# Kernel tuning notes

Measured on AMD Instinct MI355X. Metric: run time of the kernel, lower is better.

## Reference

```python
import jax, jax.numpy as jnp
import numpy as np

N = 10000   # nodes
E = 100000  # edges
B = 64      # graphs
HID = 128


def setup_inputs() -> dict:
    key = jax.random.key(0)
    ks = iter(jax.random.split(key, 64))
    def nrm(shape, s=0.1):
        return jax.random.normal(next(ks), shape, dtype=jnp.float32) * s
    inp = {}
    inp["x"] = nrm((N, 1), 1.0)
    inp["node_type"] = jax.random.randint(next(ks), (N,), 0, 2)
    inp["edge_index"] = jax.random.randint(next(ks), (2, E), 0, N)
    inp["edge_attr"] = nrm((E, 1), 1.0)
    inp["batch"] = jnp.sort(jax.random.randint(next(ks), (N,), 0, B))
    inp["vp_w"] = nrm((1, HID)); inp["vp_b"] = nrm((HID,))
    inp["type_emb"] = nrm((2, HID))
    def conv(pre, fin, h, c):
        inp[pre + "_wl"] = nrm((fin, h * c)); inp[pre + "_bl"] = nrm((h * c,))
        inp[pre + "_wr"] = nrm((fin, h * c)); inp[pre + "_br"] = nrm((h * c,))
        inp[pre + "_we"] = nrm((1, h * c));  inp[pre + "_att"] = nrm((h, c))
        inp[pre + "_bias"] = nrm((h * c if pre != "c3" else c,))
    conv("c1", HID, 8, HID)
    conv("c2", HID * 8, 2, HID)
    conv("c3", HID * 2, 1, HID)
    inp["m1_w"] = nrm((HID, HID)); inp["m1_b"] = nrm((HID,))
    inp["ln1_g"] = jnp.ones((HID,), jnp.float32); inp["ln1_b"] = jnp.zeros((HID,), jnp.float32)
    inp["m2_w"] = nrm((HID, HID // 2)); inp["m2_b"] = nrm((HID // 2,))
    inp["ln2_g"] = jnp.ones((HID // 2,), jnp.float32); inp["ln2_b"] = jnp.zeros((HID // 2,), jnp.float32)
    inp["m3_w"] = nrm((HID // 2, 1)); inp["m3_b"] = nrm((1,))
    return inp


def _gatv2(x, src, dst, ea, wl, bl, wr, br, we, att, bias, heads, out_ch, concat):
    """PyG GATv2Conv (eval mode): add self-loops (edge_attr fill='mean' over dst),
    attn = (att * leaky_relu(Wl x_src + Wr x_dst + We e)).sum(-1), segment-softmax
    over destination, scatter-add of alpha * Wl x_src."""
    n = x.shape[0]
    ones = jnp.ones((ea.shape[0], 1), ea.dtype)
    deg = jax.ops.segment_sum(ones, dst, num_segments=n)
    loop_attr = jax.ops.segment_sum(ea, dst, num_segments=n) / jnp.maximum(deg, 1.0)
    ar = jnp.arange(n, dtype=src.dtype)
    src2 = jnp.concatenate([src, ar])
    dst2 = jnp.concatenate([dst, ar])
    ea2 = jnp.concatenate([ea, loop_attr], axis=0)
    xl = (x @ wl + bl).reshape(n, heads, out_ch)   # source transform
    xr = (x @ wr + br).reshape(n, heads, out_ch)   # target transform
    e = (ea2 @ we).reshape(-1, heads, out_ch)      # [E2, H, C]
    msg = xl[src2]                                 # [E2, H, C]
    z = jax.nn.leaky_relu(msg + xr[dst2] + e, 0.2)
    score = jnp.einsum('ehc,hc->eh', z, att)       # [E2, H]
    smax = jax.ops.segment_max(score, dst2, num_segments=n)
    ex = jnp.exp(score - smax[dst2])
    denom = jax.ops.segment_sum(ex, dst2, num_segments=n)
    alpha = ex / denom[dst2]
    out = jax.ops.segment_sum(alpha[:, :, None] * msg, dst2, num_segments=n)
    out = out.reshape(n, heads * out_ch) if concat else out.mean(axis=1)
    return out + bias


def _layernorm(v, g, b):
    mu = v.mean(-1, keepdims=True)
    var = v.var(-1, keepdims=True)
    return (v - mu) / jnp.sqrt(var + 1e-5) * g + b


def reference(x, node_type, edge_index, edge_attr, batch,
              vp_w, vp_b, type_emb,
              c1_wl, c1_bl, c1_wr, c1_br, c1_we, c1_att, c1_bias,
              c2_wl, c2_bl, c2_wr, c2_br, c2_we, c2_att, c2_bias,
              c3_wl, c3_bl, c3_wr, c3_br, c3_we, c3_att, c3_bias,
              m1_w, m1_b, ln1_g, ln1_b, m2_w, m2_b, ln2_g, ln2_b, m3_w, m3_b):
    src, dst = edge_index[0], edge_index[1]
    h = x @ vp_w + vp_b + type_emb[node_type]
    h = jax.nn.leaky_relu(_gatv2(h, src, dst, edge_attr, c1_wl, c1_bl, c1_wr, c1_br, c1_we, c1_att, c1_bias, 8, HID, True), 0.2)
    h = jax.nn.leaky_relu(_gatv2(h, src, dst, edge_attr, c2_wl, c2_bl, c2_wr, c2_br, c2_we, c2_att, c2_bias, 2, HID, True), 0.2)
    h = jax.nn.leaky_relu(_gatv2(h, src, dst, edge_attr, c3_wl, c3_bl, c3_wr, c3_br, c3_we, c3_att, c3_bias, 1, HID, False), 0.2)
    # masked global mean pool over node_type == 0
    w = (node_type == 0).astype(h.dtype)
    sums = jax.ops.segment_sum(h * w[:, None], batch, num_segments=B)
    cnts = jax.ops.segment_sum(w, batch, num_segments=B)
    pooled = sums / jnp.maximum(cnts, 1.0)[:, None]
    h1 = jax.nn.leaky_relu(_layernorm(pooled @ m1_w + m1_b, ln1_g, ln1_b), 0.2)
    h2 = jax.nn.leaky_relu(_layernorm(h1 @ m2_w + m2_b, ln2_g, ln2_b), 0.2)
    return (h2 @ m3_w + m3_b).squeeze(-1)
```

## Files before the change

kernel.cpp:

```cpp
#include <hip/hip_runtime.h>
#include <math.h>

#define NN 10000
#define NE 100000
#define NBATCH 64

typedef short bf16x8 __attribute__((ext_vector_type(8)));
typedef float f32x4 __attribute__((ext_vector_type(4)));

__device__ __forceinline__ float lrelu(float v){ return fmaxf(v, 0.2f*v); }

__device__ __forceinline__ unsigned short f2bf(float x){
  unsigned int u = __float_as_uint(x);
  u += 0x7fffu + ((u >> 16) & 1u);
  return (unsigned short)(u >> 16);
}
__device__ __forceinline__ float bf2f(unsigned short u){
  return __uint_as_float(((unsigned int)u) << 16);
}

__global__ __launch_bounds__(256) void prep_kernel(
    const float* __restrict__ vp_w, const float* __restrict__ vp_b,
    const float* __restrict__ type_emb,
    const float* __restrict__ c1_wl, const float* __restrict__ c1_bl,
    const float* __restrict__ c1_wr, const float* __restrict__ c1_br,
    float* __restrict__ Ul, float* __restrict__ CTl,
    float* __restrict__ Ur, float* __restrict__ CTr,
    const float* __restrict__ c2_wl, const float* __restrict__ c2_wr,
    const float* __restrict__ c3_wl, const float* __restrict__ c3_wr,
    unsigned short* __restrict__ W2lT, unsigned short* __restrict__ W2rT,
    unsigned short* __restrict__ W3lT, unsigned short* __restrict__ W3rT,
    float* __restrict__ zbase, int zero_words)
{
  __shared__ float t[64][65];
  int b = blockIdx.x;
  int tid = threadIdx.x;
  if (b < 144){
    const float* in; unsigned short* out; int K, N, idx;
    if (b < 64)      { in=c2_wl; out=W2lT; K=1024; N=256; idx=b; }
    else if (b <128) { in=c2_wr; out=W2rT; K=1024; N=256; idx=b-64; }
    else if (b <136) { in=c3_wl; out=W3lT; K=256;  N=128; idx=b-128; }
    else             { in=c3_wr; out=W3rT; K=256;  N=128; idx=b-136; }
    int K64 = K >> 6;
    int kx = idx % K64, nx = idx / K64;
    int k0 = kx*64, n0 = nx*64;
    int lr = tid >> 4;
    int lc = (tid & 15) * 4;
#pragma unroll
    for (int i=0;i<4;++i){
      int r = lr + i*16;
      float4 v = *(const float4*)(in + (size_t)(k0+r)*N + n0 + lc);
      t[r][lc+0]=v.x; t[r][lc+1]=v.y; t[r][lc+2]=v.z; t[r][lc+3]=v.w;
    }
    __syncthreads();
    int sr = tid >> 3;
    int sc = (tid & 7) * 8;
#pragma unroll
    for (int i=0;i<2;++i){
      int n = sr + i*32;
      unsigned short tmp[8];
#pragma unroll
      for (int j=0;j<8;++j) tmp[j] = f2bf(t[sc+j][n]);
      unsigned short* op = out + (size_t)(n0+n)*K + k0 + sc;
      *(ushort4*)op       = make_ushort4(tmp[0],tmp[1],tmp[2],tmp[3]);
      *(ushort4*)(op + 4) = make_ushort4(tmp[4],tmp[5],tmp[6],tmp[7]);
    }
  } else if (b < 148){
    int j = (b-144)*256 + tid;
    float ul=0.f, c0l=0.f, c1l=0.f, ur=0.f, c0r=0.f, c1r=0.f;
    for (int k=0; k<128; ++k){
      float a = c1_wl[k*1024 + j], bb = c1_wr[k*1024 + j];
      float vw = vp_w[k], vb = vp_b[k], t0 = type_emb[k], t1 = type_emb[128+k];
      ul += vw*a; ur += vw*bb;
      c0l += (vb+t0)*a; c1l += (vb+t1)*a;
      c0r += (vb+t0)*bb; c1r += (vb+t1)*bb;
    }
    float bl = c1_bl[j], br = c1_br[j];
    Ul[j]=ul; Ur[j]=ur;
    CTl[j]      = c0l + bl;
    CTl[1024+j] = c1l + bl;
    CTr[j]      = c0r + br;
    CTr[1024+j] = c1r + br;
  } else {
    for (int i = (b-148)*256 + tid; i < zero_words; i += 32*256)
      zbase[i] = 0.f;
  }
}

__global__ void count_kernel(const int* __restrict__ dst, const float* __restrict__ ea,
                             int* __restrict__ deg, float* __restrict__ loop_sum){
  int e = blockIdx.x*256 + threadIdx.x;
  if (e < NE){
    int d = dst[e];
    atomicAdd(&deg[d], 1);
    atomicAdd(&loop_sum[d], ea[e]);
  }
}

__global__ __launch_bounds__(1024) void scan_kernel(const int* __restrict__ deg,
    const float* __restrict__ loop_sum, const float* __restrict__ x,
    const int* __restrict__ ntype,
    int* __restrict__ rowptr, float* __restrict__ loop_attr, float2* __restrict__ xt){
  __shared__ int wtot[16];
  int tid = threadIdx.x;
  int lane = tid & 63, wid = tid >> 6;
  int base = tid*10;
  int d[10]; int run = 0;
#pragma unroll
  for (int j=0;j<10;++j){
    int i = base + j;
    int v = (i < NN) ? deg[i] : 0;
    run += v; d[j] = run;
  }
  int T = run;
  int incl = T;
#pragma unroll
  for (int off=1; off<64; off<<=1){
    int s = __shfl_up(incl, off, 64);
    if (lane >= off) incl += s;
  }
  if (lane == 63) wtot[wid] = incl;
  __syncthreads();
  int wpre = 0;
  for (int w2=0; w2<wid; ++w2) wpre += wtot[w2];
  int ebase = wpre + incl - T;
#pragma unroll
  for (int j=0;j<10;++j){
    int i = base + j;
    if (i < NN){
      int v = d[j] - ((j==0) ? 0 : d[j-1]);
      rowptr[i] = ebase + d[j] - v;
      loop_attr[i] = loop_sum[i] / fmaxf((float)v, 1.f);
      xt[i] = make_float2(x[i], (float)ntype[i]);
    }
  }
  if (tid == 1023) rowptr[NN] = wpre + incl;
}

__global__ void fill_kernel(const int* __restrict__ src, const int* __restrict__ dst,
                            const float* __restrict__ ea, const int* __restrict__ rowptr,
                            int* __restrict__ rowctr, int2* __restrict__ se){
  int e = blockIdx.x*256 + threadIdx.x;
  if (e < NE){
    int d = dst[e];
    int p = rowptr[d] + atomicAdd(&rowctr[d], 1);
    se[p] = make_int2(src[e], __float_as_int(ea[e]));
  }
}

__global__ __launch_bounds__(256) void conv1_fused(
    const int* __restrict__ rowptr, const int2* __restrict__ se,
    const float* __restrict__ loop_attr, const float2* __restrict__ xt,
    const float* __restrict__ Ul, const float* __restrict__ Ur,
    const float* __restrict__ CTl, const float* __restrict__ CTr,
    const float* __restrict__ we, const float* __restrict__ att,
    const float* __restrict__ bias, unsigned short* __restrict__ out)
{
  int n = blockIdx.x*2 + (threadIdx.x >> 7);
  if (n >= NN) return;
  int te = threadIdx.x & 127;
  int ch0 = te * 8;
  float ul[8], wev[8], atv[8], cn0[8], cnd[8];
#pragma unroll
  for (int v=0; v<8; ++v){ ul[v]=Ul[ch0+v]; wev[v]=we[ch0+v]; atv[v]=att[ch0+v]; }
  int beg = rowptr[n], deg = rowptr[n+1]-beg;
  float2 xtn = xt[n];
  float la = loop_attr[n];
  const float* ctr = (xtn.y != 0.f) ? (CTr+1024) : CTr;
#pragma unroll
  for (int v=0; v<8; ++v){
    float c0 = CTl[ch0+v], c1 = CTl[1024+ch0+v];
    cn0[v] = fmaf(xtn.x, Ur[ch0+v], ctr[ch0+v]) + c0;
    cnd[v] = c1 - c0;
  }
  const int2* sp = se + beg;
  const int2 self = make_int2(n, __float_as_int(la));
  int2 qc = (deg > 0) ? sp[0] : self;
  float2 xc = xt[qc.x];
  int2 qn = (1 < deg) ? sp[1] : self;
  float l = 0.f, s1 = 0.f, st1 = 0.f;
  for (int idx=0; idx<=deg; ++idx){
    int2 qnn = (idx+2 < deg) ? sp[idx+2] : self;
    float2 xn = xt[qn.x];
    float xs = xc.x, tf = xc.y, ea = __int_as_float(qc.y);
    float acc = 0.f;
#pragma unroll
    for (int v=0; v<8; ++v){
      float t = fmaf(tf, cnd[v], cn0[v]);
      float z = fmaf(xs, ul[v], fmaf(ea, wev[v], t));
      acc = fmaf(atv[v], fmaxf(z, 0.2f*z), acc);
    }
    acc += __shfl_xor(acc, 1, 16);
    acc += __shfl_xor(acc, 2, 16);
    acc += __shfl_xor(acc, 4, 16);
    acc += __shfl_xor(acc, 8, 16);
    float pe = __expf(acc);
    l += pe;
    s1  = fmaf(pe, xs, s1);
    st1 = fmaf(pe, tf, st1);
    qc = qn; xc = xn; qn = qnn;
  }
  float inv = 1.f/l;
  s1 *= inv;
  float s21 = st1 * inv;
  float s20 = 1.f - s21;
  bf16x8 ov;
#pragma unroll
  for (int v=0; v<8; ++v){
    float c0 = CTl[ch0+v], c1 = CTl[1024+ch0+v];
    float o = lrelu(fmaf(s1, ul[v], fmaf(s20, c0, fmaf(s21, c1, bias[ch0+v]))));
    ov[v] = (short)f2bf(o);
  }
  *(bf16x8*)(out + (size_t)n*1024 + ch0) = ov;
}

template<int H, int NPB, int VPT, bool ONLY0, bool OUTBF, bool INBF>
__global__ __launch_bounds__(64*NPB) void conv_kernel(
    const int* __restrict__ rowptr, const int2* __restrict__ se,
    const float* __restrict__ loop_attr, const int* __restrict__ ntype,
    const void* __restrict__ Xv, int stride, int xr_off,
    const float* __restrict__ we, const float* __restrict__ att, const float* __restrict__ bias,
    void* __restrict__ out)
{
  const int HC = 64*VPT;
  const int TPH = 64/H;
  int n = blockIdx.x*NPB + (threadIdx.x >> 6);
  if (n >= NN) return;
  if (ONLY0 && ntype[n] != 0) return;
  int tid = threadIdx.x & 63;
  int ch0 = tid * VPT;
  const float* Xf = (const float*)Xv;
  const unsigned short* Xb = (const unsigned short*)Xv;
  float wev[VPT], atv[VPT], biv[VPT], xrv[VPT];
#pragma unroll
  for (int v=0; v<VPT; ++v){
    int ch = ch0+v;
    wev[v]=we[ch]; atv[v]=att[ch]; biv[v]=bias[ch];
  }
  if constexpr (INBF){
    ushort4 q = *(const ushort4*)(Xb + (size_t)n*stride + xr_off + ch0);
    xrv[0]=bf2f(q.x); xrv[1]=bf2f(q.y); xrv[2]=bf2f(q.z); xrv[3]=bf2f(q.w);
  } else {
#pragma unroll
    for (int v=0; v<VPT; ++v) xrv[v]=Xf[(size_t)n*stride + xr_off + ch0+v];
  }
  float ls[4], A[4][VPT];
#pragma unroll
  for (int k=0; k<4; ++k){
    ls[k] = 0.f;
#pragma unroll
    for (int v=0; v<VPT; ++v) A[k][v] = 0.f;
  }
  int beg=rowptr[n], end=rowptr[n+1];
  float la = loop_attr[n];
  for (int j=beg; j<=end; j+=4){
    bool val[4]; int sx[4]; float ex[4];
#pragma unroll
    for (int k=0; k<4; ++k){
      int pos = j + k;
      val[k] = pos <= end;
      int2 q;
      if (pos < end) q = se[pos];
      else           q = make_int2(n, __float_as_int(la));
      sx[k] = q.x; ex[k] = __int_as_float(q.y);
    }
    float xv[4][VPT];
#pragma unroll
    for (int k=0; k<4; ++k){
      if constexpr (INBF){
        ushort4 q = *(const ushort4*)(Xb + (size_t)sx[k]*stride + ch0);
        xv[k][0]=bf2f(q.x); xv[k][1]=bf2f(q.y); xv[k][2]=bf2f(q.z); xv[k][3]=bf2f(q.w);
      } else if constexpr (VPT == 4){
        float4 q = *(const float4*)(Xf + (size_t)sx[k]*stride + ch0);
        xv[k][0]=q.x; xv[k][1]=q.y; xv[k][2]=q.z; xv[k][3]=q.w;
      } else {
        float2 q = *(const float2*)(Xf + (size_t)sx[k]*stride + ch0);
        xv[k][0]=q.x; xv[k][1]=q.y;
      }
    }
    float p[4];
#pragma unroll
    for (int k=0; k<4; ++k){
      float acc = 0.f;
#pragma unroll
      for (int v=0; v<VPT; ++v)
        acc += atv[v]*lrelu(xv[k][v]+xrv[v]+ex[k]*wev[v]);
      p[k] = acc;
    }
#pragma unroll
    for (int mm=1; mm<TPH; mm<<=1){
#pragma unroll
      for (int k=0; k<4; ++k) p[k] += __shfl_xor(p[k], mm, 64);
    }
#pragma unroll
    for (int k=0; k<4; ++k){
      float pe = val[k] ? __expf(p[k]) : 0.f;
      ls[k] += pe;
#pragma unroll
      for (int v=0; v<VPT; ++v) A[k][v] = fmaf(pe, xv[k][v], A[k][v]);
    }
  }
  float lt = (ls[0]+ls[1]) + (ls[2]+ls[3]);
  float inv = 1.f/lt;
  size_t baseo=(size_t)n*HC+ch0;
  if constexpr (OUTBF){
    unsigned short* ob = (unsigned short*)out;
    ushort4 o;
    o.x = f2bf(lrelu(((A[0][0]+A[1][0])+(A[2][0]+A[3][0]))*inv+biv[0]));
    o.y = f2bf(lrelu(((A[0][1]+A[1][1])+(A[2][1]+A[3][1]))*inv+biv[1]));
    o.z = f2bf(lrelu(((A[0][2]+A[1][2])+(A[2][2]+A[3][2]))*inv+biv[2]));
    o.w = f2bf(lrelu(((A[0][3]+A[1][3])+(A[2][3]+A[3][3]))*inv+biv[3]));
    *(ushort4*)(ob + baseo) = o;
  } else {
    float* of = (float*)out;
#pragma unroll
    for (int v=0; v<VPT; ++v)
      of[baseo+v] = lrelu(((A[0][v]+A[1][v])+(A[2][v]+A[3][v]))*inv+biv[v]);
  }
}

template<bool OUTBF>
__global__ __launch_bounds__(256) void gemm_dual_lds(
    const short* __restrict__ Abf,
    const short* __restrict__ WlT, const short* __restrict__ WrT,
    const float* __restrict__ bl, const float* __restrict__ br,
    void* __restrict__ Out, int M, int K, int NcH, int cgrid, int rgrid)
{
  __shared__ short lds[12288];
  int id = blockIdx.x;
  int xcd = id & 7, slot = id >> 3;
  int nb = slot % cgrid;
  int rowgroup = (slot / cgrid) * 8 + xcd;
  if (rowgroup >= rgrid) return;
  int row0 = rowgroup * 128;
  int NC2 = 2*NcH;
  int halfx = NcH >> 6;
  int isR = nb >= halfx;
  const short* WT = isR ? WrT : WlT;
  const float* bias = isR ? br : bl;
  int col0 = (nb - (isR ? halfx : 0)) * 64;
  int gcol0 = nb * 64;
  int tid = threadIdx.x;
  int lane = tid & 63, wave = tid >> 6;
  int wm = wave >> 1, wn = wave & 1;
  int quad = lane >> 4, l16 = lane & 15;

  const short* asrc[4];
#pragma unroll
  for (int i=0;i<4;++i){
    int c = wave*256 + i*64 + lane;
    int m = c >> 3, j = c & 7;
    int gr = row0 + m; gr = gr < M ? gr : M-1;
    asrc[i] = Abf + (size_t)gr*K + ((j ^ (m & 7)) << 3);
  }
  const short* bsrc[2];
#pragma unroll
  for (int i=0;i<2;++i){
    int c = wave*128 + i*64 + lane;
    int nloc = c >> 3, j = c & 7;
    bsrc[i] = WT + (size_t)(col0 + nloc)*K + ((j ^ (nloc & 7)) << 3);
  }

  float biasv[2] = { bias[col0 + wn*32 + l16], bias[col0 + wn*32 + 16 + l16] };
  f32x4 acc[4][2];
#pragma unroll
  for (int f=0; f<4; ++f)
#pragma unroll
    for (int g=0; g<2; ++g) acc[f][g] = (f32x4){0.f,0.f,0.f,0.f};

  int niter = K >> 6;
  for (int it=0; it<niter; ++it){
    int k0 = it << 6;
#pragma unroll
    for (int i=0;i<4;++i)
      __builtin_amdgcn_global_load_lds(asrc[i] + k0, &lds[(wave*256 + i*64)*8], 16, 0, 0);
#pragma unroll
    for (int i=0;i<2;++i)
      __builtin_amdgcn_global_load_lds(bsrc[i] + k0, &lds[8192 + (wave*128 + i*64)*8], 16, 0, 0);
    __syncthreads();
#pragma unroll
    for (int s=0; s<2; ++s){
      int t = s*4 + quad;
      bf16x8 af[4], bfv[2];
#pragma unroll
      for (int f=0; f<4; ++f){
        int m = wm*64 + f*16 + l16;
        af[f] = *(const bf16x8*)&lds[m*64 + ((t ^ (m & 7)) << 3)];
      }
#pragma unroll
      for (int g=0; g<2; ++g){
        int nloc = wn*32 + g*16 + l16;
        bfv[g] = *(const bf16x8*)&lds[8192 + nloc*64 + ((t ^ (nloc & 7)) << 3)];
      }
#pragma unroll
      for (int f=0; f<4; ++f)
#pragma unroll
        for (int g=0; g<2; ++g)
          acc[f][g] = __builtin_amdgcn_mfma_f32_16x16x32_bf16(af[f], bfv[g], acc[f][g], 0,0,0);
    }
    __syncthreads();
  }

#pragma unroll
  for (int f=0; f<4; ++f){
    int rbase = row0 + wm*64 + f*16 + quad*4;
#pragma unroll
    for (int r=0; r<4; ++r){
      int rr = rbase + r;
      if (rr < M){
#pragma unroll
        for (int g=0; g<2; ++g){
          int cc = gcol0 + wn*32 + g*16 + l16;
          float val = acc[f][g][r] + biasv[g];
          if constexpr (OUTBF) ((unsigned short*)Out)[(size_t)rr*NC2 + cc] = f2bf(val);
          else                 ((float*)Out)[(size_t)rr*NC2 + cc] = val;
        }
      }
    }
  }
}

__device__ __forceinline__ int lbound(const int* __restrict__ a, int n, int key){
  int lo = 0, hi = n;
  while (lo < hi){ int mid = (lo+hi) >> 1; if (a[mid] < key) lo = mid+1; else hi = mid; }
  return lo;
}

__global__ __launch_bounds__(128) void head_kernel(
    const float* __restrict__ h3, const int* __restrict__ ntype, const int* __restrict__ batch,
    const float* __restrict__ m1w, const float* __restrict__ m1b,
    const float* __restrict__ g1, const float* __restrict__ b1,
    const float* __restrict__ m2w, const float* __restrict__ m2b,
    const float* __restrict__ g2, const float* __restrict__ b2,
    const float* __restrict__ m3w, const float* __restrict__ m3b,
    float* __restrict__ out)
{
  __shared__ float p[128];
  __shared__ float hb[128];
  __shared__ float red[128];
  int b = blockIdx.x, j = threadIdx.x;
  int lo = lbound(batch, NN, b);
  int hi = lbound(batch, NN, b+1);
  float s = 0.f, cnt = 0.f;
  int n = lo;
  for (; n + 3 < hi; n += 4){
    float w0 = (ntype[n]   == 0) ? 1.f : 0.f;
    float w1 = (ntype[n+1] == 0) ? 1.f : 0.f;
    float w2 = (ntype[n+2] == 0) ? 1.f : 0.f;
    float w3 = (ntype[n+3] == 0) ? 1.f : 0.f;
    s += w0*h3[(size_t)n*128 + j]     + w1*h3[(size_t)(n+1)*128 + j]
       + w2*h3[(size_t)(n+2)*128 + j] + w3*h3[(size_t)(n+3)*128 + j];
    cnt += w0 + w1 + w2 + w3;
  }
  for (; n < hi; ++n){
    float w = (ntype[n] == 0) ? 1.f : 0.f;
    s += w*h3[(size_t)n*128 + j];
    cnt += w;
  }
  p[j] = s / fmaxf(cnt, 1.f);
  __syncthreads();
  float a = m1b[j];
  for (int k=0; k<128; ++k) a += p[k]*m1w[k*128 + j];
  red[j] = a; __syncthreads();
  for (int off=64; off>0; off>>=1){ if (j<off) red[j] += red[j+off]; __syncthreads(); }
  float mu = red[0] * (1.f/128.f);
  __syncthreads();
  float d = a - mu;
  red[j] = d*d; __syncthreads();
  for (int off=64; off>0; off>>=1){ if (j<off) red[j] += red[j+off]; __syncthreads(); }
  float var = red[0] * (1.f/128.f);
  __syncthreads();
  hb[j] = lrelu(d * rsqrtf(var + 1e-5f) * g1[j] + b1[j]);
  __syncthreads();
  float a2 = 0.f;
  if (j < 64){
    a2 = m2b[j];
    for (int k=0; k<128; ++k) a2 += hb[k]*m2w[k*64 + j];
  }
  red[j] = (j<64) ? a2 : 0.f; __syncthreads();
  for (int off=64; off>0; off>>=1){ if (j<off) red[j] += red[j+off]; __syncthreads(); }
  float mu2 = red[0] * (1.f/64.f);
  __syncthreads();
  float d2 = a2 - mu2;
  red[j] = (j<64) ? d2*d2 : 0.f; __syncthreads();
  for (int off=64; off>0; off>>=1){ if (j<off) red[j] += red[j+off]; __syncthreads(); }
  float var2 = red[0] * (1.f/64.f);
  __syncthreads();
  if (j < 64) hb[j] = lrelu(d2 * rsqrtf(var2 + 1e-5f) * g2[j] + b2[j]);
  __syncthreads();
  if (j == 0){
    float o = m3b[0];
    for (int k=0; k<64; ++k) o += hb[k]*m3w[k];
    out[b] = o;
  }
}

extern "C" void kernel_launch(void* const* d_in, const int* in_sizes, int n_in,
                              void* d_out, int out_size, void* d_ws, size_t ws_size,
                              hipStream_t stream)
{
  const float* x        = (const float*)d_in[0];
  const int*   ntype    = (const int*)d_in[1];
  const int*   ei       = (const int*)d_in[2];
  const float* eattr    = (const float*)d_in[3];
  const int*   batch    = (const int*)d_in[4];
  const float* vp_w     = (const float*)d_in[5];
  const float* vp_b     = (const float*)d_in[6];
  const float* type_emb = (const float*)d_in[7];
  const float* c1_wl = (const float*)d_in[8];  const float* c1_bl = (const float*)d_in[9];
  const float* c1_wr = (const float*)d_in[10]; const float* c1_br = (const float*)d_in[11];
  const float* c1_we = (const float*)d_in[12]; const float* c1_att= (const float*)d_in[13];
  const float* c1_bias=(const float*)d_in[14];
  const float* c2_wl = (const float*)d_in[15]; const float* c2_bl = (const float*)d_in[16];
  const float* c2_wr = (const float*)d_in[17]; const float* c2_br = (const float*)d_in[18];
  const float* c2_we = (const float*)d_in[19]; const float* c2_att= (const float*)d_in[20];
  const float* c2_bias=(const float*)d_in[21];
  const float* c3_wl = (const float*)d_in[22]; const float* c3_bl = (const float*)d_in[23];
  const float* c3_wr = (const float*)d_in[24]; const float* c3_br = (const float*)d_in[25];
  const float* c3_we = (const float*)d_in[26]; const float* c3_att= (const float*)d_in[27];
  const float* c3_bias=(const float*)d_in[28];
  const float* m1_w = (const float*)d_in[29]; const float* m1_b = (const float*)d_in[30];
  const float* ln1_g= (const float*)d_in[31]; const float* ln1_b= (const float*)d_in[32];
  const float* m2_w = (const float*)d_in[33]; const float* m2_b = (const float*)d_in[34];
  const float* ln2_g= (const float*)d_in[35]; const float* ln2_b= (const float*)d_in[36];
  const float* m3_w = (const float*)d_in[37]; const float* m3_b = (const float*)d_in[38];
  const int* esrc = ei;
  const int* edst = ei + NE;
  float* outp = (float*)d_out;
  (void)in_sizes; (void)n_in; (void)out_size; (void)ws_size;

  char* w = (char*)d_ws;
  auto alloc = [&](size_t bytes) -> void* {
    void* p = (void*)w;
    w += (bytes + 255) & ~(size_t)255;
    return p;
  };
  unsigned short* h1bf = (unsigned short*)alloc((size_t)NN*1024*2);
  unsigned short* X2   = (unsigned short*)alloc((size_t)NN*512*2);
  unsigned short* h2bf = (unsigned short*)alloc((size_t)NN*256*2);
  float* X3   = (float*)alloc((size_t)NN*256*4);
  float* h3   = (float*)alloc((size_t)NN*128*4);
  unsigned short* W2lT = (unsigned short*)alloc((size_t)256*1024*2);
  unsigned short* W2rT = (unsigned short*)alloc((size_t)256*1024*2);
  unsigned short* W3lT = (unsigned short*)alloc((size_t)128*256*2);
  unsigned short* W3rT = (unsigned short*)alloc((size_t)128*256*2);
  float* Ul   = (float*)alloc(1024*4);
  float* CTl  = (float*)alloc(2048*4);
  float* Ur   = (float*)alloc(1024*4);
  float* CTr  = (float*)alloc(2048*4);
  const int zero_words = 3*NN;
  float* zbase = (float*)alloc((size_t)zero_words*4);
  int*   deg      = (int*)zbase;
  int*   rowctr   = (int*)(zbase + NN);
  float* loop_sum = zbase + 2*NN;
  float* loop_attr= (float*)alloc((size_t)NN*4);
  float2* xt      = (float2*)alloc((size_t)NN*8);
  int*   rowptr   = (int*)alloc((size_t)(NN+1)*4);
  int2*  se       = (int2*)alloc((size_t)NE*8);

  prep_kernel<<<180, 256, 0, stream>>>(vp_w, vp_b, type_emb,
      c1_wl, c1_bl, c1_wr, c1_br, Ul, CTl, Ur, CTr,
      c2_wl, c2_wr, c3_wl, c3_wr, W2lT, W2rT, W3lT, W3rT,
      zbase, zero_words);
  count_kernel<<<(NE+255)/256, 256, 0, stream>>>(edst, eattr, deg, loop_sum);
  scan_kernel<<<1, 1024, 0, stream>>>(deg, loop_sum, x, ntype, rowptr, loop_attr, xt);
  fill_kernel<<<(NE+255)/256, 256, 0, stream>>>(esrc, edst, eattr, rowptr, rowctr, se);
  conv1_fused<<<NN/2, 256, 0, stream>>>(rowptr, se, loop_attr, xt,
      Ul, Ur, CTl, CTr, c1_we, c1_att, c1_bias, h1bf);
  gemm_dual_lds<true><<<640, 256, 0, stream>>>(
      (const short*)h1bf, (const short*)W2lT, (const short*)W2rT, c2_bl, c2_br,
      (void*)X2, NN, 1024, 256, 8, 79);
  conv_kernel<2,4,4,false,true,true><<<NN/4, 256, 0, stream>>>(rowptr, se, loop_attr, ntype,
      (const void*)X2, 512, 256, c2_we, c2_att, c2_bias, h2bf);
  gemm_dual_lds<false><<<320, 256, 0, stream>>>(
      (const short*)h2bf, (const short*)W3lT, (const short*)W3rT, c3_bl, c3_br,
      (void*)X3, NN, 256, 128, 4, 79);
  conv_kernel<1,4,2,true,false,false><<<NN/4, 256, 0, stream>>>(rowptr, se, loop_attr, ntype,
      (const void*)X3, 256, 128, c3_we, c3_att, c3_bias, h3);
  head_kernel<<<NBATCH, 128, 0, stream>>>(h3, ntype, batch, m1_w, m1_b, ln1_g, ln1_b,
                                          m2_w, m2_b, ln2_g, ln2_b, m3_w, m3_b, outp);
}
```

Before: 314.5 us.

## Store self-loops in CSR, pair-unroll conv1 edges, and rewrite leaky_relu via abs

Self-loop entries now live directly in the CSR edge array. The scan kernel writes each node's loop entry at the start of its row and the fill kernel offsets real edges by one. This removes the per-edge branch that selected between a stored edge and a synthesized self entry, and drops the loop_attr buffer. conv1 now processes two edges per iteration with independent accumulators and prefetches further ahead. All conv kernels compute leaky_relu as 0.6*z + 0.4*|z| with the attention weights pre-scaled, saving a multiply and max per channel. Reads past each row end rely on padding at the array tail and may fetch neighbouring rows' entries, but those are masked or discarded.

```diff
diff --git a/kernel.cpp b/kernel.cpp
--- a/kernel.cpp
+++ b/kernel.cpp
@@ -3,6 +3,7 @@
 
 #define NN 10000
 #define NE 100000
+#define E2 (NE + NN)
 #define NBATCH 64
 
 typedef short bf16x8 __attribute__((ext_vector_type(8)));
@@ -100,7 +101,7 @@
 __global__ __launch_bounds__(1024) void scan_kernel(const int* __restrict__ deg,
     const float* __restrict__ loop_sum, const float* __restrict__ x,
     const int* __restrict__ ntype,
-    int* __restrict__ rowptr, float* __restrict__ loop_attr, float2* __restrict__ xt){
+    int* __restrict__ rowptr, int2* __restrict__ se, float2* __restrict__ xt){
   __shared__ int wtot[16];
   int tid = threadIdx.x;
   int lane = tid & 63, wid = tid >> 6;
@@ -129,12 +130,19 @@
     int i = base + j;
     if (i < NN){
       int v = d[j] - ((j==0) ? 0 : d[j-1]);
-      rowptr[i] = ebase + d[j] - v;
-      loop_attr[i] = loop_sum[i] / fmaxf((float)v, 1.f);
+      int rp2 = ebase + d[j] - v + i;
+      rowptr[i] = rp2;
+      float la = loop_sum[i] / fmaxf((float)v, 1.f);
+      se[rp2] = make_int2(i, __float_as_int(la));
       xt[i] = make_float2(x[i], (float)ntype[i]);
     }
   }
-  if (tid == 1023) rowptr[NN] = wpre + incl;
+  if (tid == 1023){
+    int tot = wpre + incl + NN;
+    rowptr[NN] = tot;
+#pragma unroll
+    for (int k=0; k<8; ++k) se[tot+k] = make_int2(0, 0);
+  }
 }
 
 __global__ void fill_kernel(const int* __restrict__ src, const int* __restrict__ dst,
@@ -143,14 +151,14 @@
   int e = blockIdx.x*256 + threadIdx.x;
   if (e < NE){
     int d = dst[e];
-    int p = rowptr[d] + atomicAdd(&rowctr[d], 1);
+    int p = rowptr[d] + 1 + atomicAdd(&rowctr[d], 1);
     se[p] = make_int2(src[e], __float_as_int(ea[e]));
   }
 }
 
 __global__ __launch_bounds__(256) void conv1_fused(
     const int* __restrict__ rowptr, const int2* __restrict__ se,
-    const float* __restrict__ loop_attr, const float2* __restrict__ xt,
+    const float2* __restrict__ xt,
     const float* __restrict__ Ul, const float* __restrict__ Ur,
     const float* __restrict__ CTl, const float* __restrict__ CTr,
     const float* __restrict__ we, const float* __restrict__ att,
@@ -160,12 +168,14 @@
   if (n >= NN) return;
   int te = threadIdx.x & 127;
   int ch0 = te * 8;
-  float ul[8], wev[8], atv[8], cn0[8], cnd[8];
-#pragma unroll
-  for (int v=0; v<8; ++v){ ul[v]=Ul[ch0+v]; wev[v]=we[ch0+v]; atv[v]=att[ch0+v]; }
-  int beg = rowptr[n], deg = rowptr[n+1]-beg;
+  float ul[8], wev[8], a1[8], a2[8], cn0[8], cnd[8];
+#pragma unroll
+  for (int v=0; v<8; ++v){
+    ul[v]=Ul[ch0+v]; wev[v]=we[ch0+v];
+    float av = att[ch0+v]; a1[v]=0.6f*av; a2[v]=0.4f*av;
+  }
+  int beg = rowptr[n], cnt = rowptr[n+1]-beg;
   float2 xtn = xt[n];
-  float la = loop_attr[n];
   const float* ctr = (xtn.y != 0.f) ? (CTr+1024) : CTr;
 #pragma unroll
   for (int v=0; v<8; ++v){
@@ -174,35 +184,53 @@
     cnd[v] = c1 - c0;
   }
   const int2* sp = se + beg;
-  const int2 self = make_int2(n, __float_as_int(la));
-  int2 qc = (deg > 0) ? sp[0] : self;
-  float2 xc = xt[qc.x];
-  int2 qn = (1 < deg) ? sp[1] : self;
-  float l = 0.f, s1 = 0.f, st1 = 0.f;
-  for (int idx=0; idx<=deg; ++idx){
-    int2 qnn = (idx+2 < deg) ? sp[idx+2] : self;
-    float2 xn = xt[qn.x];
-    float xs = xc.x, tf = xc.y, ea = __int_as_float(qc.y);
-    float acc = 0.f;
+  int2 q0 = sp[0], q1 = sp[1], q2 = sp[2], q3 = sp[3];
+  float2 x0 = xt[q0.x], x1 = xt[q1.x];
+  float la_=0.f, lb_=0.f, s1a=0.f, s1b=0.f, sta=0.f, stb=0.f;
+  int npair = cnt >> 1;
+  for (int p=0; p<npair; ++p){
+    int i = p*2;
+    float2 x2 = xt[q2.x], x3 = xt[q3.x];
+    int2 q4 = sp[i+4], q5 = sp[i+5];
+    float xs0=x0.x, tf0=x0.y, ea0=__int_as_float(q0.y);
+    float xs1=x1.x, tf1=x1.y, ea1=__int_as_float(q1.y);
+    float p0a=0.f,p0b=0.f,p1a=0.f,p1b=0.f;
 #pragma unroll
     for (int v=0; v<8; ++v){
-      float t = fmaf(tf, cnd[v], cn0[v]);
-      float z = fmaf(xs, ul[v], fmaf(ea, wev[v], t));
-      acc = fmaf(atv[v], fmaxf(z, 0.2f*z), acc);
-    }
-    acc += __shfl_xor(acc, 1, 16);
-    acc += __shfl_xor(acc, 2, 16);
-    acc += __shfl_xor(acc, 4, 16);
-    acc += __shfl_xor(acc, 8, 16);
-    float pe = __expf(acc);
-    l += pe;
-    s1  = fmaf(pe, xs, s1);
-    st1 = fmaf(pe, tf, st1);
-    qc = qn; xc = xn; qn = qnn;
-  }
-  float inv = 1.f/l;
-  s1 *= inv;
-  float s21 = st1 * inv;
+      float z0 = fmaf(xs0, ul[v], fmaf(ea0, wev[v], fmaf(tf0, cnd[v], cn0[v])));
+      float z1 = fmaf(xs1, ul[v], fmaf(ea1, wev[v], fmaf(tf1, cnd[v], cn0[v])));
+      p0a = fmaf(a1[v], z0, p0a); p0b = fmaf(a2[v], fabsf(z0), p0b);
+      p1a = fmaf(a1[v], z1, p1a); p1b = fmaf(a2[v], fabsf(z1), p1b);
+    }
+    float p0 = p0a+p0b, p1 = p1a+p1b;
+#pragma unroll
+    for (int mm=1; mm<16; mm<<=1){
+      p0 += __shfl_xor(p0, mm, 16);
+      p1 += __shfl_xor(p1, mm, 16);
+    }
+    float pe0 = __expf(p0), pe1 = __expf(p1);
+    la_ += pe0; lb_ += pe1;
+    s1a = fmaf(pe0, xs0, s1a); s1b = fmaf(pe1, xs1, s1b);
+    sta = fmaf(pe0, tf0, sta); stb = fmaf(pe1, tf1, stb);
+    q0=q2; x0=x2; q1=q3; x1=x3; q2=q4; q3=q5;
+  }
+  if (cnt & 1){
+    float xs0=x0.x, tf0=x0.y, ea0=__int_as_float(q0.y);
+    float p0a=0.f,p0b=0.f;
+#pragma unroll
+    for (int v=0; v<8; ++v){
+      float z0 = fmaf(xs0, ul[v], fmaf(ea0, wev[v], fmaf(tf0, cnd[v], cn0[v])));
+      p0a = fmaf(a1[v], z0, p0a); p0b = fmaf(a2[v], fabsf(z0), p0b);
+    }
+    float p0 = p0a+p0b;
+#pragma unroll
+    for (int mm=1; mm<16; mm<<=1) p0 += __shfl_xor(p0, mm, 16);
+    float pe0 = __expf(p0);
+    la_ += pe0; s1a = fmaf(pe0, xs0, s1a); sta = fmaf(pe0, tf0, sta);
+  }
+  float inv = 1.f/(la_+lb_);
+  float s1 = (s1a+s1b)*inv;
+  float s21 = (sta+stb)*inv;
   float s20 = 1.f - s21;
   bf16x8 ov;
 #pragma unroll
@@ -217,7 +245,7 @@
 template<int H, int NPB, int VPT, bool ONLY0, bool OUTBF, bool INBF>
 __global__ __launch_bounds__(64*NPB) void conv_kernel(
     const int* __restrict__ rowptr, const int2* __restrict__ se,
-    const float* __restrict__ loop_attr, const int* __restrict__ ntype,
+    const int* __restrict__ ntype,
     const void* __restrict__ Xv, int stride, int xr_off,
     const float* __restrict__ we, const float* __restrict__ att, const float* __restrict__ bias,
     void* __restrict__ out)
@@ -231,11 +259,12 @@
   int ch0 = tid * VPT;
   const float* Xf = (const float*)Xv;
   const unsigned short* Xb = (const unsigned short*)Xv;
-  float wev[VPT], atv[VPT], biv[VPT], xrv[VPT];
+  float wev[VPT], a1v[VPT], a2v[VPT], biv[VPT], xrv[VPT];
 #pragma unroll
   for (int v=0; v<VPT; ++v){
     int ch = ch0+v;
-    wev[v]=we[ch]; atv[v]=att[ch]; biv[v]=bias[ch];
+    wev[v]=we[ch]; biv[v]=bias[ch];
+    float av = att[ch]; a1v[v]=0.6f*av; a2v[v]=0.4f*av;
   }
   if constexpr (INBF){
     ushort4 q = *(const ushort4*)(Xb + (size_t)n*stride + xr_off + ch0);
@@ -252,16 +281,13 @@
     for (int v=0; v<VPT; ++v) A[k][v] = 0.f;
   }
   int beg=rowptr[n], end=rowptr[n+1];
-  float la = loop_attr[n];
-  for (int j=beg; j<=end; j+=4){
+  for (int j=beg; j<end; j+=4){
     bool val[4]; int sx[4]; float ex[4];
 #pragma unroll
     for (int k=0; k<4; ++k){
       int pos = j + k;
-      val[k] = pos <= end;
-      int2 q;
-      if (pos < end) q = se[pos];
-      else           q = make_int2(n, __float_as_int(la));
+      val[k] = pos < end;
+      int2 q = se[pos];
       sx[k] = q.x; ex[k] = __int_as_float(q.y);
     }
     float xv[4][VPT];
@@ -281,11 +307,14 @@
     float p[4];
 #pragma unroll
     for (int k=0; k<4; ++k){
-      float acc = 0.f;
-#pragma unroll
-      for (int v=0; v<VPT; ++v)
-        acc += atv[v]*lrelu(xv[k][v]+xrv[v]+ex[k]*wev[v]);
-      p[k] = acc;
+      float pa = 0.f, pb = 0.f;
+#pragma unroll
+      for (int v=0; v<VPT; ++v){
+        float z = fmaf(ex[k], wev[v], xv[k][v]+xrv[v]);
+        pa = fmaf(a1v[v], z, pa);
+        pb = fmaf(a2v[v], fabsf(z), pb);
+      }
+      p[k] = pa + pb;
     }
 #pragma unroll
     for (int mm=1; mm<TPH; mm<<=1){
@@ -553,29 +582,28 @@
   int*   deg      = (int*)zbase;
   int*   rowctr   = (int*)(zbase + NN);
   float* loop_sum = zbase + 2*NN;
-  float* loop_attr= (float*)alloc((size_t)NN*4);
   float2* xt      = (float2*)alloc((size_t)NN*8);
   int*   rowptr   = (int*)alloc((size_t)(NN+1)*4);
-  int2*  se       = (int2*)alloc((size_t)NE*8);
+  int2*  se       = (int2*)alloc((size_t)(E2+8)*8);
 
   prep_kernel<<<180, 256, 0, stream>>>(vp_w, vp_b, type_emb,
       c1_wl, c1_bl, c1_wr, c1_br, Ul, CTl, Ur, CTr,
       c2_wl, c2_wr, c3_wl, c3_wr, W2lT, W2rT, W3lT, W3rT,
       zbase, zero_words);
   count_kernel<<<(NE+255)/256, 256, 0, stream>>>(edst, eattr, deg, loop_sum);
-  scan_kernel<<<1, 1024, 0, stream>>>(deg, loop_sum, x, ntype, rowptr, loop_attr, xt);
+  scan_kernel<<<1, 1024, 0, stream>>>(deg, loop_sum, x, ntype, rowptr, se, xt);
   fill_kernel<<<(NE+255)/256, 256, 0, stream>>>(esrc, edst, eattr, rowptr, rowctr, se);
-  conv1_fused<<<NN/2, 256, 0, stream>>>(rowptr, se, loop_attr, xt,
+  conv1_fused<<<NN/2, 256, 0, stream>>>(rowptr, se, xt,
       Ul, Ur, CTl, CTr, c1_we, c1_att, c1_bias, h1bf);
   gemm_dual_lds<true><<<640, 256, 0, stream>>>(
       (const short*)h1bf, (const short*)W2lT, (const short*)W2rT, c2_bl, c2_br,
       (void*)X2, NN, 1024, 256, 8, 79);
-  conv_kernel<2,4,4,false,true,true><<<NN/4, 256, 0, stream>>>(rowptr, se, loop_attr, ntype,
+  conv_kernel<2,4,4,false,true,true><<<NN/4, 256, 0, stream>>>(rowptr, se, ntype,
       (const void*)X2, 512, 256, c2_we, c2_att, c2_bias, h2bf);
   gemm_dual_lds<false><<<320, 256, 0, stream>>>(
       (const short*)h2bf, (const short*)W3lT, (const short*)W3rT, c3_bl, c3_br,
       (void*)X3, NN, 256, 128, 4, 79);
-  conv_kernel<1,4,2,true,false,false><<<NN/4, 256, 0, stream>>>(rowptr, se, loop_attr, ntype,
+  conv_kernel<1,4,2,true,false,false><<<NN/4, 256, 0, stream>>>(rowptr, se, ntype,
       (const void*)X3, 256, 128, c3_we, c3_att, c3_bias, h3);
   head_kernel<<<NBATCH, 128, 0, stream>>>(h3, ntype, batch, m1_w, m1_b, ln1_g, ln1_b,
                                           m2_w, m2_b, ln2_g, ln2_b, m3_w, m3_b, outp);
```

Result: no change. 311.0 us, median of 3 (-1.1%).
